# Kernel optimization log

Hardware: AMD Instinct MI355X
Metric: run time of the kernel (lower is better)

Reference implementation:

```python
import jax, jax.numpy as jnp
import numpy as np

NQ = 23          # number of qubits -> statevector dim 2**23
NC = 23          # circuit width used by config_circuit_fun
NUM_BLOCK = 1    # number of repeated blocks


def _config_circuit(nc, nq, num_block):
    # UID 0 = parametrized single-qubit gate, UID 1 = CNOT
    uid_block = [0] * nc + [1] * (nc - 1)
    qid_block = list(range(nc))
    for q in range(nc - 1):
        # qubitID_fun(q0=q, q1=q+1, Nq) = q*(Nq-1) + (q+1-q-1) % Nq = q*(Nq-1)
        qid_block.append(q * (nq - 1))
    return uid_block * num_block, qid_block * num_block


def _u3(theta):
    # General single-qubit gate U = Rz(a) @ Ry(b) @ Rz(c), theta = (a, b, c)
    a = theta[0].astype(jnp.complex64)
    c = theta[2].astype(jnp.complex64)
    cb = jnp.cos(theta[1] * 0.5).astype(jnp.complex64)
    sb = jnp.sin(theta[1] * 0.5).astype(jnp.complex64)
    ea, eA = jnp.exp(-0.5j * a), jnp.exp(0.5j * a)
    ec, eC = jnp.exp(-0.5j * c), jnp.exp(0.5j * c)
    row0 = jnp.stack([ea * cb * ec, -ea * sb * eC])
    row1 = jnp.stack([eA * sb * ec, eA * cb * eC])
    return jnp.stack([row0, row1])  # (2, 2) complex64


def _apply1(U, q, state):
    # apply 2x2 gate U on qubit q of statevector (length 2**NQ)
    st = state.reshape(2 ** q, 2, -1)
    return jnp.einsum('ij,ajb->aib', U, st).reshape(-1)


def _apply2(U4, q0, q1, state):
    # apply 4x4 gate on qubits (q0, q1), q0 < q1
    st = state.reshape(2 ** q0, 2, 2 ** (q1 - q0 - 1), 2, -1)
    Ut = U4.reshape(2, 2, 2, 2)  # (out0, out1, in0, in1)
    return jnp.einsum('ijkl,akblc->aibjc', Ut, st).reshape(-1)


def setup_inputs() -> dict:
    key = jax.random.key(0)
    k1, k2, k3 = jax.random.split(key, 3)
    depth = (2 * NC - 1) * NUM_BLOCK
    param = jax.random.normal(k1, (depth * 3,), dtype=jnp.float32)
    re = jax.random.normal(k2, (2 ** NQ,), dtype=jnp.float32)
    im = jax.random.normal(k3, (2 ** NQ,), dtype=jnp.float32)
    nrm = jnp.sqrt(jnp.sum(re * re + im * im))
    return {"state_re": re / nrm, "state_im": im / nrm, "param": param}


def reference(state_re, state_im, param):
    uids, qids = _config_circuit(NC, NQ, NUM_BLOCK)
    depth = len(uids)
    th = param.reshape(depth, 3)
    cnot = jnp.array([[1, 0, 0, 0],
                      [0, 1, 0, 0],
                      [0, 0, 0, 1],
                      [0, 0, 1, 0]], dtype=jnp.complex64)
    state = (state_re + 1j * state_im).astype(jnp.complex64)
    for i in range(depth):
        if uids[i] == 0:
            state = _apply1(_u3(th[i]), qids[i], state)
        else:
            q0 = qids[i] // (NQ - 1)
            q1 = (qids[i] - q0 * (NQ - 1) + q0 + 1) % NQ
            state = _apply2(cnot, q0, q1, state)
    # return real/imag stacked (schema has no complex dtype)
    return jnp.stack([jnp.real(state), jnp.imag(state)])
```

## Files before the change

kernel.cpp:

```cpp
#include <hip/hip_runtime.h>
#include <math.h>


#define NTOT (1u << 23)

typedef unsigned int u2 __attribute__((ext_vector_type(2)));

struct G8 { float r00,i00,r01,i01,r10,i10,r11,i11; };

__device__ __forceinline__ G8 u3_lane(const float* __restrict__ p, int q) {
    float a = p[3*q+0], b = p[3*q+1], c = p[3*q+2];
    float cb = cosf(b*0.5f), sb = sinf(b*0.5f);
    float ph = (a+c)*0.5f, m = (a-c)*0.5f;
    float cp = cosf(ph), sp = sinf(ph);
    float cm = cosf(m),  sm = sinf(m);
    G8 g;
    g.r00 =  cb*cp; g.i00 = -cb*sp;
    g.r01 = -sb*cm; g.i01 =  sb*sm;
    g.r10 =  sb*cm; g.i10 =  sb*sm;
    g.r11 =  cb*cp; g.i11 =  cb*sp;
    return g;
}

__device__ __forceinline__ float rdl(float v, int q) {
    return __uint_as_float(__builtin_amdgcn_readlane(__float_as_uint(v), q));
}
__device__ __forceinline__ G8 gread(const G8& m, int q) {
    G8 g;
    g.r00=rdl(m.r00,q); g.i00=rdl(m.i00,q);
    g.r01=rdl(m.r01,q); g.i01=rdl(m.i01,q);
    g.r10=rdl(m.r10,q); g.i10=rdl(m.i10,q);
    g.r11=rdl(m.r11,q); g.i11=rdl(m.i11,q);
    return g;
}

__device__ __forceinline__ void bfs(float& x0r, float& x0i, float& x1r, float& x1i, const G8& g) {
    float y0r = g.r00*x0r - g.i00*x0i + g.r01*x1r - g.i01*x1i;
    float y0i = g.r00*x0i + g.i00*x0r + g.r01*x1i + g.i01*x1r;
    float y1r = g.r10*x0r - g.i10*x0i + g.r11*x1r - g.i11*x1i;
    float y1i = g.r10*x0i + g.i10*x0r + g.r11*x1i + g.i11*x1r;
    x0r=y0r; x0i=y0i; x1r=y1r; x1i=y1i;
}
__device__ __forceinline__ void bf4v(float4& ar, float4& ai, float4& br, float4& bi, const G8& g) {
    bfs(ar.x, ai.x, br.x, bi.x, g);
    bfs(ar.y, ai.y, br.y, bi.y, g);
    bfs(ar.z, ai.z, br.z, bi.z, g);
    bfs(ar.w, ai.w, br.w, bi.w, g);
}
__device__ __forceinline__ void bfc0(float4& r, float4& i, const G8& g) {
    bfs(r.x, i.x, r.y, i.y, g); bfs(r.z, i.z, r.w, i.w, g);
}
__device__ __forceinline__ void bfc1(float4& r, float4& i, const G8& g) {
    bfs(r.x, i.x, r.z, i.z, g); bfs(r.y, i.y, r.w, i.w, g);
}
__device__ __forceinline__ void reg_gate0(float4 (&xr)[4], float4 (&xi)[4], const G8& g) {
    bf4v(xr[0],xi[0],xr[1],xi[1],g); bf4v(xr[2],xi[2],xr[3],xi[3],g);
}
__device__ __forceinline__ void reg_gate1(float4 (&xr)[4], float4 (&xi)[4], const G8& g) {
    bf4v(xr[0],xi[0],xr[2],xi[2],g); bf4v(xr[1],xi[1],xr[3],xi[3],g);
}

__device__ __forceinline__ float p_dpp1(float x) {
    return __uint_as_float((unsigned)__builtin_amdgcn_update_dpp(
        0, (int)__float_as_uint(x), 0xB1, 0xF, 0xF, true));
}
__device__ __forceinline__ float p_dpp2(float x) {
    return __uint_as_float((unsigned)__builtin_amdgcn_update_dpp(
        0, (int)__float_as_uint(x), 0x4E, 0xF, 0xF, true));
}
__device__ __forceinline__ float p_x16(float x, int hi) {
#if __has_builtin(__builtin_amdgcn_permlane16_swap)
    u2 r = __builtin_amdgcn_permlane16_swap(__float_as_uint(x), __float_as_uint(x), false, false);
    return __uint_as_float(hi ? r[0] : r[1]);
#else
    (void)hi;
    return __uint_as_float((unsigned)__builtin_amdgcn_ds_swizzle(
        (int)__float_as_uint(x), 0x401F));
#endif
}
__device__ __forceinline__ float p_x32(float x, int hi) {
#if __has_builtin(__builtin_amdgcn_permlane32_swap)
    u2 r = __builtin_amdgcn_permlane32_swap(__float_as_uint(x), __float_as_uint(x), false, false);
    return __uint_as_float(hi ? r[0] : r[1]);
#else
    (void)hi;
    return __shfl_xor(x, 32, 64);
#endif
}

__device__ __forceinline__ void pcomb(float4 (&xr)[4], float4 (&xi)[4],
                                      const float4 (&pr)[4], const float4 (&pi)[4],
                                      const G8& g, int bit) {
    float cor = bit ? g.r11 : g.r00, coi = bit ? g.i11 : g.i00;
    float cpr = bit ? g.r10 : g.r01, cpi = bit ? g.i10 : g.i01;
#pragma unroll
    for (int i = 0; i < 4; ++i) {
        float4 nr, ni;
        nr.x = cor*xr[i].x - coi*xi[i].x + cpr*pr[i].x - cpi*pi[i].x;
        ni.x = cor*xi[i].x + coi*xr[i].x + cpr*pi[i].x + cpi*pr[i].x;
        nr.y = cor*xr[i].y - coi*xi[i].y + cpr*pr[i].y - cpi*pi[i].y;
        ni.y = cor*xi[i].y + coi*xr[i].y + cpr*pi[i].y + cpi*pr[i].y;
        nr.z = cor*xr[i].z - coi*xi[i].z + cpr*pr[i].z - cpi*pi[i].z;
        ni.z = cor*xi[i].z + coi*xr[i].z + cpr*pi[i].z + cpi*pr[i].z;
        nr.w = cor*xr[i].w - coi*xi[i].w + cpr*pr[i].w - cpi*pi[i].w;
        ni.w = cor*xi[i].w + coi*xr[i].w + cpr*pi[i].w + cpi*pr[i].w;
        xr[i] = nr; xi[i] = ni;
    }
}

#define MAKE_PGATE(NAME, FETCH)                                                     \
__device__ __forceinline__ void NAME(float4 (&xr)[4], float4 (&xi)[4],              \
                                     const G8& g, int bit, int hi) {                \
    float4 pr[4], pi[4];                                                            \
    _Pragma("unroll")                                                               \
    for (int i = 0; i < 4; ++i) {                                                   \
        pr[i].x = FETCH(xr[i].x); pr[i].y = FETCH(xr[i].y);                         \
        pr[i].z = FETCH(xr[i].z); pr[i].w = FETCH(xr[i].w);                         \
        pi[i].x = FETCH(xi[i].x); pi[i].y = FETCH(xi[i].y);                         \
        pi[i].z = FETCH(xi[i].z); pi[i].w = FETCH(xi[i].w);                         \
    }                                                                               \
    (void)hi; pcomb(xr, xi, pr, pi, g, bit);                                        \
}
#define F_DPP1(v) p_dpp1(v)
#define F_DPP2(v) p_dpp2(v)
#define F_X16(v)  p_x16(v, hi)
#define F_X32(v)  p_x32(v, hi)
MAKE_PGATE(gate_dpp1, F_DPP1)
MAKE_PGATE(gate_dpp2, F_DPP2)
MAKE_PGATE(gate_x16,  F_X16)
MAKE_PGATE(gate_x32,  F_X32)

__device__ __forceinline__ int pxor12(int x) { x^=x>>1; x^=x>>2; x^=x>>4; x^=x>>8; return x & 0xFFF; }
__device__ __forceinline__ int pxor9(int x)  { x^=x>>1; x^=x>>2; x^=x>>4; x^=x>>8; return x & 0x1FF; }

__global__ __launch_bounds__(1024)
void pass_high(const float* __restrict__ in_re, const float* __restrict__ in_im,
               const float* __restrict__ param,
               float* __restrict__ out_re, float* __restrict__ out_im) {
    __shared__ __align__(16) char L[131072];
    const int tid = threadIdx.x, blk = blockIdx.x;
    const int l = tid & 63, w = tid >> 6;
    G8 my = u3_lane(param, l < 23 ? l : 22);
    float4 xr[4], xi[4];

    const float4* R4p = (const float4*)in_re;
    const float4* I4p = (const float4*)in_im;
    const int rb = (l >> 3) | (w << 5);
    const size_t gb0 = ((size_t)blk << 3) | (size_t)(l & 7);
#pragma unroll
    for (int j = 0; j < 4; ++j) {
        size_t gi = (((size_t)(rb | (j << 3))) << 12) | gb0;
        xr[j] = R4p[gi]; xi[j] = I4p[gi];
    }
    const int b1  = l & 1;
    const int h16 = (l >> 4) & 1, h32 = (l >> 5) & 1;

    { G8 g = gread(my,22);
#pragma unroll
      for (int j = 0; j < 4; ++j) bfc0(xr[j], xi[j], g); }
    { G8 g = gread(my,21);
#pragma unroll
      for (int j = 0; j < 4; ++j) bfc1(xr[j], xi[j], g); }
    { G8 g = gread(my,5); reg_gate0(xr, xi, g); }
    { G8 g = gread(my,4); reg_gate1(xr, xi, g); }
    { G8 g = gread(my,7); gate_x16(xr, xi, g, h16, h16); }
    { G8 g = gread(my,6); gate_x32(xr, xi, g, h32, h32); }

#pragma unroll
    for (int j = 0; j < 4; ++j) {
        int a = ((w << 8) | (j << 6) | l) << 4;
        *(float4*)(L + a) = xr[j];
        *(float4*)(L + a + 65536) = xi[j];
    }
    __syncthreads();
    const int sbase = ((l >> 1) & 7) | ((w & 3) << 4) | (((w >> 2) & 3) << 6)
                    | (((l >> 4) & 3) << 9) | ((l & 1) << 11);
    constexpr int OFF[4] = {0, 8, 256, 264};
#pragma unroll
    for (int j = 0; j < 4; ++j) {
        int a = (sbase | OFF[j]) << 4;
        xr[j] = *(const float4*)(L + a);
        xi[j] = *(const float4*)(L + a + 65536);
    }

    { G8 g = gread(my,8); reg_gate0(xr, xi, g); }
    { G8 g = gread(my,3); reg_gate1(xr, xi, g); }
    { G8 g = gread(my,0); gate_dpp1(xr, xi, g, b1, 0); }
    { G8 g = gread(my,2); gate_x16(xr, xi, g, h16, h16); }
    { G8 g = gread(my,1); gate_x32(xr, xi, g, h32, h32); }

    float4* OR4 = (float4*)out_re;
    float4* OI4 = (float4*)out_im;
    const int row_base = ((w & 15) << 1) | (((l >> 4) & 3) << 6) | ((l & 1) << 8);
    const int sg = pxor9(row_base);
    const size_t ob = ((size_t)blk << 3) | (size_t)((l >> 1) & 7);
    constexpr int SJ[4] = {0, 0x01, 0x3F, 0x3E};
#pragma unroll
    for (int j = 0; j < 4; ++j) {
        size_t F = (((size_t)(sg ^ SJ[j])) << 12) | ob;
        OR4[F] = xr[j]; OI4[F] = xi[j];
    }
}

__global__ __launch_bounds__(1024)
void pass_low(float* __restrict__ sre, float* __restrict__ sim,
              const float* __restrict__ param) {
    __shared__ __align__(16) char L[131072];
    const int tid = threadIdx.x, c = blockIdx.x;
    const int l = tid & 63, w = tid >> 6;
    G8 my = u3_lane(param, l < 23 ? l : 22);
    float4 xr[4], xi[4];

    float4* R4p = (float4*)sre;
    float4* I4p = (float4*)sim;
    const size_t cb = ((size_t)c) << 12;
    const int sw0 = (w << 8) | l;
#pragma unroll
    for (int j = 0; j < 4; ++j) {
        size_t fi = cb + (size_t)(sw0 | (j << 6));
        xr[j] = R4p[fi]; xi[j] = I4p[fi];
    }
    const int b1 = l & 1, b2 = (l >> 1) & 1;
    const int h16 = (l >> 4) & 1, h32 = (l >> 5) & 1;

    { G8 g = gread(my,20); gate_dpp1(xr, xi, g, b1, 0); }
    { G8 g = gread(my,19); gate_dpp2(xr, xi, g, b2, 0); }
    { G8 g = gread(my,16); gate_x16(xr, xi, g, h16, h16); }
    { G8 g = gread(my,15); gate_x32(xr, xi, g, h32, h32); }
    { G8 g = gread(my,14); reg_gate0(xr, xi, g); }
    { G8 g = gread(my,13); reg_gate1(xr, xi, g); }

#pragma unroll
    for (int j = 0; j < 4; ++j) {
        int a = (sw0 | (j << 6)) << 4;
        *(float4*)(L + a) = xr[j];
        *(float4*)(L + a + 65536) = xi[j];
    }
    __syncthreads();
    const int sbase = ((l >> 2) & 3) | ((l & 3) << 2) | ((w & 15) << 4) | (((l >> 4) & 3) << 10);
#pragma unroll
    for (int j = 0; j < 4; ++j) {
        int a = (sbase | (j << 8)) << 4;
        xr[j] = *(const float4*)(L + a);
        xi[j] = *(const float4*)(L + a + 65536);
    }

    { G8 g = gread(my,18); gate_dpp1(xr, xi, g, b1, 0); }
    { G8 g = gread(my,17); gate_dpp2(xr, xi, g, b2, 0); }
    { G8 g = gread(my,12); reg_gate0(xr, xi, g); }
    { G8 g = gread(my,11); reg_gate1(xr, xi, g); }
    { G8 g = gread(my,10); gate_x16(xr, xi, g, h16, h16); }
    { G8 g = gread(my, 9); gate_x32(xr, xi, g, h32, h32); }

    const int px0 = pxor12(sbase);
    const int codd = c & 1;
    const int A12 = codd ? 0xFFF : 0;
    constexpr int PM[4] = {0, 0x1FF, 0x3FF, 0x200};
#pragma unroll
    for (int j = 0; j < 4; ++j) {
        int pxj = px0 ^ PM[j];
        int of4 = pxj ^ A12;
        int b = (pxj ^ codd) & 1;
        float s0r = xr[j].x, s1r = xr[j].y, s2r = xr[j].w, s3r = xr[j].z;
        float s0i = xi[j].x, s1i = xi[j].y, s2i = xi[j].w, s3i = xi[j].z;
        float o0r = b ? s3r : s0r, o1r = b ? s2r : s1r, o2r = b ? s1r : s2r, o3r = b ? s0r : s3r;
        float o0i = b ? s3i : s0i, o1i = b ? s2i : s1i, o2i = b ? s1i : s2i, o3i = b ? s0i : s3i;
        size_t oo = cb | (size_t)of4;
        R4p[oo] = make_float4(o0r, o1r, o2r, o3r);
        I4p[oo] = make_float4(o0i, o1i, o2i, o3i);
    }
}

extern "C" void kernel_launch(void* const* d_in, const int* in_sizes, int n_in,
                              void* d_out, int out_size, void* d_ws, size_t ws_size,
                              hipStream_t stream) {
    (void)in_sizes; (void)n_in; (void)d_ws; (void)ws_size; (void)out_size;
    const float* in_re = (const float*)d_in[0];
    const float* in_im = (const float*)d_in[1];
    const float* param = (const float*)d_in[2];
    float* out_re = (float*)d_out;
    float* out_im = (float*)d_out + NTOT;

    pass_high<<<512, 1024, 0, stream>>>(in_re, in_im, param, out_re, out_im);
    pass_low <<<512, 1024, 0, stream>>>(out_re, out_im, param);
}
```

Baseline: 77.14 us.

## Process two tiles per block with both tiles' global loads issued upfront

Each block of both passes now handles two tiles (blockIdx and blockIdx+256) and launches half as many blocks. Both tiles' global loads are issued before any compute, so the second tile's memory latency hides behind the first tile's gates and shared-memory shuffle. The permute-gate macro is also fused so each float4's partner fetch and combine happen in one loop iteration, which lowers live registers. This roughly doubles per-thread register pressure for the held tiles, adds an extra barrier per tile, and leaves only 256 blocks to cover the device's CUs, with one 128KB-LDS block per CU.

```diff
diff --git a/kernel.cpp b/kernel.cpp
--- a/kernel.cpp
+++ b/kernel.cpp
@@ -88,38 +88,29 @@
 #endif
 }
 
-__device__ __forceinline__ void pcomb(float4 (&xr)[4], float4 (&xi)[4],
-                                      const float4 (&pr)[4], const float4 (&pi)[4],
-                                      const G8& g, int bit) {
-    float cor = bit ? g.r11 : g.r00, coi = bit ? g.i11 : g.i00;
-    float cpr = bit ? g.r10 : g.r01, cpi = bit ? g.i10 : g.i01;
-#pragma unroll
-    for (int i = 0; i < 4; ++i) {
-        float4 nr, ni;
-        nr.x = cor*xr[i].x - coi*xi[i].x + cpr*pr[i].x - cpi*pi[i].x;
-        ni.x = cor*xi[i].x + coi*xr[i].x + cpr*pi[i].x + cpi*pr[i].x;
-        nr.y = cor*xr[i].y - coi*xi[i].y + cpr*pr[i].y - cpi*pi[i].y;
-        ni.y = cor*xi[i].y + coi*xr[i].y + cpr*pi[i].y + cpi*pr[i].y;
-        nr.z = cor*xr[i].z - coi*xi[i].z + cpr*pr[i].z - cpi*pi[i].z;
-        ni.z = cor*xi[i].z + coi*xr[i].z + cpr*pi[i].z + cpi*pr[i].z;
-        nr.w = cor*xr[i].w - coi*xi[i].w + cpr*pr[i].w - cpi*pi[i].w;
-        ni.w = cor*xi[i].w + coi*xr[i].w + cpr*pi[i].w + cpi*pr[i].w;
-        xr[i] = nr; xi[i] = ni;
-    }
-}
-
 #define MAKE_PGATE(NAME, FETCH)                                                     \
 __device__ __forceinline__ void NAME(float4 (&xr)[4], float4 (&xi)[4],              \
                                      const G8& g, int bit, int hi) {                \
-    float4 pr[4], pi[4];                                                            \
+    float cor = bit ? g.r11 : g.r00, coi = bit ? g.i11 : g.i00;                     \
+    float cpr = bit ? g.r10 : g.r01, cpi = bit ? g.i10 : g.i01;                     \
+    (void)hi;                                                                       \
     _Pragma("unroll")                                                               \
     for (int i = 0; i < 4; ++i) {                                                   \
-        pr[i].x = FETCH(xr[i].x); pr[i].y = FETCH(xr[i].y);                         \
-        pr[i].z = FETCH(xr[i].z); pr[i].w = FETCH(xr[i].w);                         \
-        pi[i].x = FETCH(xi[i].x); pi[i].y = FETCH(xi[i].y);                         \
-        pi[i].z = FETCH(xi[i].z); pi[i].w = FETCH(xi[i].w);                         \
+        float4 pr, pi, nr, ni;                                                      \
+        pr.x = FETCH(xr[i].x); pr.y = FETCH(xr[i].y);                               \
+        pr.z = FETCH(xr[i].z); pr.w = FETCH(xr[i].w);                               \
+        pi.x = FETCH(xi[i].x); pi.y = FETCH(xi[i].y);                               \
+        pi.z = FETCH(xi[i].z); pi.w = FETCH(xi[i].w);                               \
+        nr.x = cor*xr[i].x - coi*xi[i].x + cpr*pr.x - cpi*pi.x;                     \
+        ni.x = cor*xi[i].x + coi*xr[i].x + cpr*pi.x + cpi*pr.x;                     \
+        nr.y = cor*xr[i].y - coi*xi[i].y + cpr*pr.y - cpi*pi.y;                     \
+        ni.y = cor*xi[i].y + coi*xr[i].y + cpr*pi.y + cpi*pr.y;                     \
+        nr.z = cor*xr[i].z - coi*xi[i].z + cpr*pr.z - cpi*pi.z;                     \
+        ni.z = cor*xi[i].z + coi*xr[i].z + cpr*pi.z + cpi*pr.z;                     \
+        nr.w = cor*xr[i].w - coi*xi[i].w + cpr*pr.w - cpi*pi.w;                     \
+        ni.w = cor*xi[i].w + coi*xr[i].w + cpr*pi.w + cpi*pr.w;                     \
+        xr[i] = nr; xi[i] = ni;                                                     \
     }                                                                               \
-    (void)hi; pcomb(xr, xi, pr, pi, g, bit);                                        \
 }
 #define F_DPP1(v) p_dpp1(v)
 #define F_DPP2(v) p_dpp2(v)
@@ -133,96 +124,96 @@
 __device__ __forceinline__ int pxor12(int x) { x^=x>>1; x^=x>>2; x^=x>>4; x^=x>>8; return x & 0xFFF; }
 __device__ __forceinline__ int pxor9(int x)  { x^=x>>1; x^=x>>2; x^=x>>4; x^=x>>8; return x & 0x1FF; }
 
+__device__ __forceinline__ void high_tile(float4 (&xr)[4], float4 (&xi)[4],
+        const G8& my, char* L, int l, int w, int blk,
+        float4* __restrict__ OR4, float4* __restrict__ OI4,
+        int b1, int h16, int h32) {
+    { G8 g = gread(my,22);
+#pragma unroll
+      for (int j = 0; j < 4; ++j) bfc0(xr[j], xi[j], g); }
+    { G8 g = gread(my,21);
+#pragma unroll
+      for (int j = 0; j < 4; ++j) bfc1(xr[j], xi[j], g); }
+    { G8 g = gread(my,5); reg_gate0(xr, xi, g); }
+    { G8 g = gread(my,4); reg_gate1(xr, xi, g); }
+    { G8 g = gread(my,7); gate_x16(xr, xi, g, h16, h16); }
+    { G8 g = gread(my,6); gate_x32(xr, xi, g, h32, h32); }
+
+    const int wslot = ((w << 8) | l) << 4;
+    const int sbase = (((l >> 1) & 7) | ((w & 3) << 4) | (((w >> 2) & 3) << 6)
+                    | (((l >> 4) & 3) << 9) | ((l & 1) << 11)) << 4;
+    constexpr int OFF[4] = {0, 8 << 4, 256 << 4, 264 << 4};
+    __syncthreads();
+#pragma unroll
+    for (int j = 0; j < 4; ++j) {
+        int a = wslot | (j << 10);
+        *(float4*)(L + a) = xr[j];
+        *(float4*)(L + a + 65536) = xi[j];
+    }
+    __syncthreads();
+#pragma unroll
+    for (int j = 0; j < 4; ++j) {
+        int a = sbase | OFF[j];
+        xr[j] = *(const float4*)(L + a);
+        xi[j] = *(const float4*)(L + a + 65536);
+    }
+
+    { G8 g = gread(my,8); reg_gate0(xr, xi, g); }
+    { G8 g = gread(my,3); reg_gate1(xr, xi, g); }
+    { G8 g = gread(my,0); gate_dpp1(xr, xi, g, b1, 0); }
+    { G8 g = gread(my,2); gate_x16(xr, xi, g, h16, h16); }
+    { G8 g = gread(my,1); gate_x32(xr, xi, g, h32, h32); }
+
+    const int row_base = ((w & 15) << 1) | (((l >> 4) & 3) << 6) | ((l & 1) << 8);
+    const int sg = pxor9(row_base);
+    const size_t ob = ((size_t)blk << 3) | (size_t)((l >> 1) & 7);
+    constexpr int SJ[4] = {0, 0x01, 0x3F, 0x3E};
+#pragma unroll
+    for (int j = 0; j < 4; ++j) {
+        size_t F = (((size_t)(sg ^ SJ[j])) << 12) | ob;
+        OR4[F] = xr[j]; OI4[F] = xi[j];
+    }
+}
+
 __global__ __launch_bounds__(1024)
 void pass_high(const float* __restrict__ in_re, const float* __restrict__ in_im,
                const float* __restrict__ param,
                float* __restrict__ out_re, float* __restrict__ out_im) {
     __shared__ __align__(16) char L[131072];
-    const int tid = threadIdx.x, blk = blockIdx.x;
+    const int tid = threadIdx.x;
     const int l = tid & 63, w = tid >> 6;
-    G8 my = u3_lane(param, l < 23 ? l : 22);
-    float4 xr[4], xi[4];
+    const int blkA = blockIdx.x, blkB = blockIdx.x + 256;
 
     const float4* R4p = (const float4*)in_re;
     const float4* I4p = (const float4*)in_im;
+    float4 ar[4], ai[4], br_[4], bi_[4];
     const int rb = (l >> 3) | (w << 5);
-    const size_t gb0 = ((size_t)blk << 3) | (size_t)(l & 7);
-#pragma unroll
-    for (int j = 0; j < 4; ++j) {
-        size_t gi = (((size_t)(rb | (j << 3))) << 12) | gb0;
-        xr[j] = R4p[gi]; xi[j] = I4p[gi];
-    }
+    const size_t gA = ((size_t)blkA << 3) | (size_t)(l & 7);
+    const size_t gB = ((size_t)blkB << 3) | (size_t)(l & 7);
+#pragma unroll
+    for (int j = 0; j < 4; ++j) {
+        size_t gi = (((size_t)(rb | (j << 3))) << 12) | gA;
+        ar[j] = R4p[gi]; ai[j] = I4p[gi];
+    }
+#pragma unroll
+    for (int j = 0; j < 4; ++j) {
+        size_t gi = (((size_t)(rb | (j << 3))) << 12) | gB;
+        br_[j] = R4p[gi]; bi_[j] = I4p[gi];
+    }
+    G8 my = u3_lane(param, l < 23 ? l : 22);
     const int b1  = l & 1;
     const int h16 = (l >> 4) & 1, h32 = (l >> 5) & 1;
 
-    { G8 g = gread(my,22);
-#pragma unroll
-      for (int j = 0; j < 4; ++j) bfc0(xr[j], xi[j], g); }
-    { G8 g = gread(my,21);
-#pragma unroll
-      for (int j = 0; j < 4; ++j) bfc1(xr[j], xi[j], g); }
-    { G8 g = gread(my,5); reg_gate0(xr, xi, g); }
-    { G8 g = gread(my,4); reg_gate1(xr, xi, g); }
-    { G8 g = gread(my,7); gate_x16(xr, xi, g, h16, h16); }
-    { G8 g = gread(my,6); gate_x32(xr, xi, g, h32, h32); }
-
-#pragma unroll
-    for (int j = 0; j < 4; ++j) {
-        int a = ((w << 8) | (j << 6) | l) << 4;
-        *(float4*)(L + a) = xr[j];
-        *(float4*)(L + a + 65536) = xi[j];
-    }
-    __syncthreads();
-    const int sbase = ((l >> 1) & 7) | ((w & 3) << 4) | (((w >> 2) & 3) << 6)
-                    | (((l >> 4) & 3) << 9) | ((l & 1) << 11);
-    constexpr int OFF[4] = {0, 8, 256, 264};
-#pragma unroll
-    for (int j = 0; j < 4; ++j) {
-        int a = (sbase | OFF[j]) << 4;
-        xr[j] = *(const float4*)(L + a);
-        xi[j] = *(const float4*)(L + a + 65536);
-    }
-
-    { G8 g = gread(my,8); reg_gate0(xr, xi, g); }
-    { G8 g = gread(my,3); reg_gate1(xr, xi, g); }
-    { G8 g = gread(my,0); gate_dpp1(xr, xi, g, b1, 0); }
-    { G8 g = gread(my,2); gate_x16(xr, xi, g, h16, h16); }
-    { G8 g = gread(my,1); gate_x32(xr, xi, g, h32, h32); }
-
     float4* OR4 = (float4*)out_re;
     float4* OI4 = (float4*)out_im;
-    const int row_base = ((w & 15) << 1) | (((l >> 4) & 3) << 6) | ((l & 1) << 8);
-    const int sg = pxor9(row_base);
-    const size_t ob = ((size_t)blk << 3) | (size_t)((l >> 1) & 7);
-    constexpr int SJ[4] = {0, 0x01, 0x3F, 0x3E};
-#pragma unroll
-    for (int j = 0; j < 4; ++j) {
-        size_t F = (((size_t)(sg ^ SJ[j])) << 12) | ob;
-        OR4[F] = xr[j]; OI4[F] = xi[j];
-    }
-}
-
-__global__ __launch_bounds__(1024)
-void pass_low(float* __restrict__ sre, float* __restrict__ sim,
-              const float* __restrict__ param) {
-    __shared__ __align__(16) char L[131072];
-    const int tid = threadIdx.x, c = blockIdx.x;
-    const int l = tid & 63, w = tid >> 6;
-    G8 my = u3_lane(param, l < 23 ? l : 22);
-    float4 xr[4], xi[4];
-
-    float4* R4p = (float4*)sre;
-    float4* I4p = (float4*)sim;
-    const size_t cb = ((size_t)c) << 12;
-    const int sw0 = (w << 8) | l;
-#pragma unroll
-    for (int j = 0; j < 4; ++j) {
-        size_t fi = cb + (size_t)(sw0 | (j << 6));
-        xr[j] = R4p[fi]; xi[j] = I4p[fi];
-    }
-    const int b1 = l & 1, b2 = (l >> 1) & 1;
-    const int h16 = (l >> 4) & 1, h32 = (l >> 5) & 1;
-
+    high_tile(ar,  ai,  my, L, l, w, blkA, OR4, OI4, b1, h16, h32);
+    high_tile(br_, bi_, my, L, l, w, blkB, OR4, OI4, b1, h16, h32);
+}
+
+__device__ __forceinline__ void low_tile(float4 (&xr)[4], float4 (&xi)[4],
+        const G8& my, char* L, int l, int w, int c,
+        float4* __restrict__ R4p, float4* __restrict__ I4p,
+        int b1, int b2, int h16, int h32) {
     { G8 g = gread(my,20); gate_dpp1(xr, xi, g, b1, 0); }
     { G8 g = gread(my,19); gate_dpp2(xr, xi, g, b2, 0); }
     { G8 g = gread(my,16); gate_x16(xr, xi, g, h16, h16); }
@@ -230,6 +221,10 @@
     { G8 g = gread(my,14); reg_gate0(xr, xi, g); }
     { G8 g = gread(my,13); reg_gate1(xr, xi, g); }
 
+    const int sw0 = (w << 8) | l;
+    const int sbase = ((l >> 2) & 3) | ((l & 3) << 2) | ((w & 15) << 4)
+                    | (((l >> 4) & 3) << 10);
+    __syncthreads();
 #pragma unroll
     for (int j = 0; j < 4; ++j) {
         int a = (sw0 | (j << 6)) << 4;
@@ -237,7 +232,6 @@
         *(float4*)(L + a + 65536) = xi[j];
     }
     __syncthreads();
-    const int sbase = ((l >> 2) & 3) | ((l & 3) << 2) | ((w & 15) << 4) | (((l >> 4) & 3) << 10);
 #pragma unroll
     for (int j = 0; j < 4; ++j) {
         int a = (sbase | (j << 8)) << 4;
@@ -252,6 +246,7 @@
     { G8 g = gread(my,10); gate_x16(xr, xi, g, h16, h16); }
     { G8 g = gread(my, 9); gate_x32(xr, xi, g, h32, h32); }
 
+    const size_t cb = ((size_t)c) << 12;
     const int px0 = pxor12(sbase);
     const int codd = c & 1;
     const int A12 = codd ? 0xFFF : 0;
@@ -271,6 +266,38 @@
     }
 }
 
+__global__ __launch_bounds__(1024)
+void pass_low(float* __restrict__ sre, float* __restrict__ sim,
+              const float* __restrict__ param) {
+    __shared__ __align__(16) char L[131072];
+    const int tid = threadIdx.x;
+    const int l = tid & 63, w = tid >> 6;
+    const int cA = blockIdx.x, cB = blockIdx.x + 256;
+
+    float4* R4p = (float4*)sre;
+    float4* I4p = (float4*)sim;
+    float4 ar[4], ai[4], br_[4], bi_[4];
+    const int sw0 = (w << 8) | l;
+    const size_t cbA = ((size_t)cA) << 12;
+    const size_t cbB = ((size_t)cB) << 12;
+#pragma unroll
+    for (int j = 0; j < 4; ++j) {
+        size_t fi = cbA + (size_t)(sw0 | (j << 6));
+        ar[j] = R4p[fi]; ai[j] = I4p[fi];
+    }
+#pragma unroll
+    for (int j = 0; j < 4; ++j) {
+        size_t fi = cbB + (size_t)(sw0 | (j << 6));
+        br_[j] = R4p[fi]; bi_[j] = I4p[fi];
+    }
+    G8 my = u3_lane(param, l < 23 ? l : 22);
+    const int b1 = l & 1, b2 = (l >> 1) & 1;
+    const int h16 = (l >> 4) & 1, h32 = (l >> 5) & 1;
+
+    low_tile(ar,  ai,  my, L, l, w, cA, R4p, I4p, b1, b2, h16, h32);
+    low_tile(br_, bi_, my, L, l, w, cB, R4p, I4p, b1, b2, h16, h32);
+}
+
 extern "C" void kernel_launch(void* const* d_in, const int* in_sizes, int n_in,
                               void* d_out, int out_size, void* d_ws, size_t ws_size,
                               hipStream_t stream) {
@@ -281,6 +308,6 @@
     float* out_re = (float*)d_out;
     float* out_im = (float*)d_out + NTOT;
 
-    pass_high<<<512, 1024, 0, stream>>>(in_re, in_im, param, out_re, out_im);
-    pass_low <<<512, 1024, 0, stream>>>(out_re, out_im, param);
-}
+    pass_high<<<256, 1024, 0, stream>>>(in_re, in_im, param, out_re, out_im);
+    pass_low <<<256, 1024, 0, stream>>>(out_re, out_im, param);
+}
```

Measured after the change: 81.46 us. 5.6% more time.
